# Kernel optimization log

Measured on AMD Instinct MI355X. Metric: run time of the kernel, lower is better.

Reference implementation:

```python
import jax, jax.numpy as jnp
import numpy as np

FP8_MAX = 448.0  # max normal of float8_e4m3fn (TE fwd format)
EPS = 1e-12


def _fp8_quant_dequant(t):
    """Per-tensor amax scaling -> cast to e4m3 -> dequant back to f32.
    Mirrors TE's per-tensor scaling recipe (scale = FP8_MAX / amax)."""
    amax = jnp.max(jnp.abs(t))
    scale = FP8_MAX / jnp.maximum(amax, EPS)
    q = jnp.clip(t * scale, -FP8_MAX, FP8_MAX).astype(jnp.float8_e4m3fn)
    return q.astype(jnp.float32) / scale


def setup_inputs() -> dict:
    key = jax.random.key(0)
    k1, k2, k3 = jax.random.split(key, 3)
    tokens, d_in, d_out = 8192, 4096, 4096
    x = jax.random.normal(k1, (tokens, d_in), dtype=jnp.float32)
    # kaiming_uniform_(a=sqrt(5)) -> U(-bound, bound), bound = sqrt(6/((1+a^2)*fan_in)) = 1/sqrt(fan_in)
    bound = 1.0 / np.sqrt(d_in)
    weight = jax.random.uniform(k2, (d_out, d_in), dtype=jnp.float32, minval=-bound, maxval=bound)
    bias = jnp.zeros((d_out,), dtype=jnp.float32) + 0.01 * jax.random.normal(k3, (d_out,), dtype=jnp.float32)
    return {"x": x, "weight": weight, "bias": bias}


def reference(x, weight, bias):
    # fp8 quant/dequant of activations and weights, then GEMM + bias
    xq = _fp8_quant_dequant(x)            # [T, Din]
    wq = _fp8_quant_dequant(weight)       # [Dout, Din]
    out = jnp.einsum("ti,oi->to", xq, wq) # [T, Dout]
    return out + bias[None, :]
```

## Files before the change

### kernel.cpp

```cpp
#include <hip/hip_runtime.h>
#include <stdint.h>

#define M_DIM 8192
#define N_DIM 4096
#define K_DIM 4096

typedef float f32x4  __attribute__((ext_vector_type(4)));
typedef float f32x16 __attribute__((ext_vector_type(16)));
typedef int   i32x4  __attribute__((ext_vector_type(4)));
typedef int   i32x8  __attribute__((ext_vector_type(8)));

__global__ __launch_bounds__(256) void amax2_kernel(const float* __restrict__ x,
                                                    const float* __restrict__ wgt,
                                                    unsigned int* __restrict__ ws_u) {
    const int which = blockIdx.y;
    const float4* p = (const float4*)(which ? wgt : x);
    const int n4 = (which ? N_DIM : M_DIM) * (K_DIM / 4);
    int tid = blockIdx.x * blockDim.x + threadIdx.x;
    int stride = gridDim.x * blockDim.x;
    float m = 0.0f;
    for (int i = tid; i < n4; i += stride) {
        float4 v = p[i];
        m = fmaxf(m, fmaxf(fmaxf(fabsf(v.x), fabsf(v.y)),
                           fmaxf(fabsf(v.z), fabsf(v.w))));
    }
#pragma unroll
    for (int off = 32; off > 0; off >>= 1)
        m = fmaxf(m, __shfl_down(m, off, 64));
    __shared__ float sm[4];
    if ((threadIdx.x & 63) == 0) sm[threadIdx.x >> 6] = m;
    __syncthreads();
    if (threadIdx.x == 0) {
        m = fmaxf(fmaxf(sm[0], sm[1]), fmaxf(sm[2], sm[3]));
        atomicMax(ws_u + which, __float_as_uint(m));
    }
}

__global__ __launch_bounds__(256) void quant2_kernel(const float* __restrict__ x,
                                                     const float* __restrict__ wgt,
                                                     unsigned int* __restrict__ xq,
                                                     unsigned int* __restrict__ wq,
                                                     const unsigned int* __restrict__ ws_u) {
    const int which = blockIdx.y;
    const float4* p = (const float4*)(which ? wgt : x);
    unsigned int* outp = which ? wq : xq;
    const int n4 = (which ? N_DIM : M_DIM) * (K_DIM / 4);
    float amax = fmaxf(__uint_as_float(ws_u[which]), 1e-12f);
    float scale = 448.0f / amax;
    int tid = blockIdx.x * blockDim.x + threadIdx.x;
    int stride = gridDim.x * blockDim.x;
    for (int i = tid; i < n4; i += stride) {
        float4 v = p[i];
        float a = fminf(fmaxf(v.x * scale, -448.0f), 448.0f);
        float b = fminf(fmaxf(v.y * scale, -448.0f), 448.0f);
        float c = fminf(fmaxf(v.z * scale, -448.0f), 448.0f);
        float d = fminf(fmaxf(v.w * scale, -448.0f), 448.0f);
        int w = __builtin_amdgcn_cvt_pk_fp8_f32(a, b, 0, false);
        w = __builtin_amdgcn_cvt_pk_fp8_f32(c, d, w, true);
        outp[i] = (unsigned int)w;
    }
}

__device__ __forceinline__ void gld16(const void* g, void* l) {
    __builtin_amdgcn_global_load_lds(
        (const __attribute__((address_space(1))) void*)g,
        (__attribute__((address_space(3))) void*)l, 16, 0, 0);
}

#define MFMA32(a, b, c) __builtin_amdgcn_mfma_scale_f32_32x32x64_f8f6f4( \
    (a), (b), (c), 0, 0, 0, 0x7F7F7F7F, 0, 0x7F7F7F7F)
#define BAR()    __builtin_amdgcn_s_barrier()
#define VMCNT(n) asm volatile("s_waitcnt vmcnt(" #n ")" ::: "memory")
#define PRIO1()  __builtin_amdgcn_s_setprio(1)
#define PRIO0()  __builtin_amdgcn_s_setprio(0)
#define FENCE()  asm volatile("" ::: "memory")

__global__ __launch_bounds__(256, 1) void gemm_fp8_kernel(
    const uint8_t* __restrict__ Aq,
    const uint8_t* __restrict__ Bq,
    const float* __restrict__ bias,
    const unsigned int* __restrict__ ws_u,
    float* __restrict__ out)
{
    __shared__ uint8_t lds[131072];

    const int tid = threadIdx.x;
    const int w = tid >> 6, l = tid & 63;

    const int cpx = (int)gridDim.x >> 3;
    const int bid = (int)blockIdx.x;
    const int swz = (bid & 7) * cpx + (bid >> 3);
    const int bm = swz >> 4, bn = swz & 15;

    const uint8_t* gA = Aq + (size_t)bm * 256 * K_DIM;
    const uint8_t* gB = Bq + (size_t)bn * 256 * K_DIM;

    const int idx = tid >> 3, p = tid & 7;
    const int srcX = ((p ^ (idx & 7)) << 4);
    const uint8_t* aRow = gA + (size_t)idx * K_DIM + srcX;
    const uint8_t* bRow = gB + (size_t)idx * K_DIM + srcX;
    const int dA = tid * 16;

    const int wr = w >> 1, wc = w & 1;
    const int lr = l & 31;
    const int hi2 = (l >> 5) << 1;
    const int rowA0 = wr * 128 + lr;
    const int rowB0 = wc * 128 + lr;

    auto stageA = [&](int bb, int kn, int half) {
#pragma unroll
        for (int r = 0; r < 4; ++r)
            gld16(aRow + (size_t)(half * 128 + r * 32) * K_DIM + kn,
                  &lds[bb * 32768 + half * 16384 + r * 4096 + dA]);
    };
    auto stageB = [&](int bb, int kn, int half) {
#pragma unroll
        for (int r = 0; r < 4; ++r)
            gld16(bRow + (size_t)(half * 128 + r * 32) * K_DIM + kn,
                  &lds[65536 + bb * 32768 + half * 16384 + r * 4096 + dA]);
    };
    auto ldf = [&](const uint8_t* base, int row, int kh) -> i32x8 {
        const uint8_t* q = base + (row << 7);
        const int rk = row & 7;
        const int c0 = (kh << 2) + hi2;
        i32x4 lo = *(const i32x4*)(q + ((c0 ^ rk) << 4));
        i32x4 hh = *(const i32x4*)(q + (((c0 + 1) ^ rk) << 4));
        return __builtin_shufflevector(lo, hh, 0, 1, 2, 3, 4, 5, 6, 7);
    };

    f32x16 acc[4][4] = {};
    i32x8 av[4], bv[4];

    stageA(0, 0, 0); stageB(0, 0, 0);
    stageA(0, 0, 1); stageB(0, 0, 1);

    for (int t = 0; t < 32; ++t) {
        const int buf = t & 1, nbuf = buf ^ 1;
        const int kn = (t + 1) * 128;
        const uint8_t* lab = &lds[buf * 32768];
        const uint8_t* lbb = &lds[65536 + buf * 32768];

        VMCNT(0);
        BAR();

        if (t < 31) { stageA(nbuf, kn, 0); stageB(nbuf, kn, 0); }
        bv[0] = ldf(lbb, rowB0, 0);      bv[1] = ldf(lbb, rowB0 + 32, 0);
        av[0] = ldf(lab, rowA0, 0);      av[1] = ldf(lab, rowA0 + 32, 0);
        av[2] = ldf(lab, rowA0 + 64, 0); av[3] = ldf(lab, rowA0 + 96, 0);
        PRIO1();
        acc[0][0] = MFMA32(av[0], bv[0], acc[0][0]);
        acc[0][1] = MFMA32(av[0], bv[1], acc[0][1]);
        acc[1][0] = MFMA32(av[1], bv[0], acc[1][0]);
        acc[1][1] = MFMA32(av[1], bv[1], acc[1][1]);
        acc[2][0] = MFMA32(av[2], bv[0], acc[2][0]);
        acc[2][1] = MFMA32(av[2], bv[1], acc[2][1]);
        acc[3][0] = MFMA32(av[3], bv[0], acc[3][0]);
        acc[3][1] = MFMA32(av[3], bv[1], acc[3][1]);
        PRIO0();
        FENCE();

        if (t < 31) { stageA(nbuf, kn, 1); stageB(nbuf, kn, 1); }
        bv[2] = ldf(lbb, rowB0 + 64, 0); bv[3] = ldf(lbb, rowB0 + 96, 0);
        PRIO1();
        acc[0][2] = MFMA32(av[0], bv[2], acc[0][2]);
        acc[0][3] = MFMA32(av[0], bv[3], acc[0][3]);
        acc[1][2] = MFMA32(av[1], bv[2], acc[1][2]);
        acc[1][3] = MFMA32(av[1], bv[3], acc[1][3]);
        acc[2][2] = MFMA32(av[2], bv[2], acc[2][2]);
        acc[2][3] = MFMA32(av[2], bv[3], acc[2][3]);
        acc[3][2] = MFMA32(av[3], bv[2], acc[3][2]);
        acc[3][3] = MFMA32(av[3], bv[3], acc[3][3]);
        PRIO0();
        FENCE();

        av[0] = ldf(lab, rowA0, 1);      av[1] = ldf(lab, rowA0 + 32, 1);
        av[2] = ldf(lab, rowA0 + 64, 1); av[3] = ldf(lab, rowA0 + 96, 1);
        bv[0] = ldf(lbb, rowB0, 1);      bv[1] = ldf(lbb, rowB0 + 32, 1);
        PRIO1();
        acc[0][0] = MFMA32(av[0], bv[0], acc[0][0]);
        acc[0][1] = MFMA32(av[0], bv[1], acc[0][1]);
        acc[1][0] = MFMA32(av[1], bv[0], acc[1][0]);
        acc[1][1] = MFMA32(av[1], bv[1], acc[1][1]);
        acc[2][0] = MFMA32(av[2], bv[0], acc[2][0]);
        acc[2][1] = MFMA32(av[2], bv[1], acc[2][1]);
        acc[3][0] = MFMA32(av[3], bv[0], acc[3][0]);
        acc[3][1] = MFMA32(av[3], bv[1], acc[3][1]);
        PRIO0();
        FENCE();

        bv[2] = ldf(lbb, rowB0 + 64, 1); bv[3] = ldf(lbb, rowB0 + 96, 1);
        PRIO1();
        acc[0][2] = MFMA32(av[0], bv[2], acc[0][2]);
        acc[0][3] = MFMA32(av[0], bv[3], acc[0][3]);
        acc[1][2] = MFMA32(av[1], bv[2], acc[1][2]);
        acc[1][3] = MFMA32(av[1], bv[3], acc[1][3]);
        acc[2][2] = MFMA32(av[2], bv[2], acc[2][2]);
        acc[2][3] = MFMA32(av[2], bv[3], acc[2][3]);
        acc[3][2] = MFMA32(av[3], bv[2], acc[3][2]);
        acc[3][3] = MFMA32(av[3], bv[3], acc[3][3]);
        PRIO0();
    }

    const float ax = fmaxf(__uint_as_float(ws_u[0]), 1e-12f);
    const float aw = fmaxf(__uint_as_float(ws_u[1]), 1e-12f);
    const float inv = (ax * (1.0f / 448.0f)) * (aw * (1.0f / 448.0f));

    const int orow0 = bm * 256 + wr * 128 + ((l >> 5) << 2);
    const int ocol0 = bn * 256 + wc * 128 + lr;
#pragma unroll
    for (int mb = 0; mb < 4; ++mb) {
#pragma unroll
        for (int nb = 0; nb < 4; ++nb) {
            const int col = ocol0 + nb * 32;
            const float bvv = bias[col];
#pragma unroll
            for (int r = 0; r < 16; ++r) {
                const int row = orow0 + mb * 32 + (r & 3) + ((r >> 2) << 3);
                out[(size_t)row * N_DIM + col] = acc[mb][nb][r] * inv + bvv;
            }
        }
    }
}

extern "C" void kernel_launch(void* const* d_in, const int* in_sizes, int n_in,
                              void* d_out, int out_size, void* d_ws, size_t ws_size,
                              hipStream_t stream) {
    const float* x    = (const float*)d_in[0];
    const float* wgt  = (const float*)d_in[1];
    const float* bias = (const float*)d_in[2];
    float* out = (float*)d_out;

    unsigned int* ws_u = (unsigned int*)d_ws;
    uint8_t* xq = (uint8_t*)d_ws + 256;
    uint8_t* wq = xq + (size_t)M_DIM * K_DIM;

    hipMemsetAsync(d_ws, 0, 8, stream);

    dim3 ga(1024, 2);
    amax2_kernel<<<ga, 256, 0, stream>>>(x, wgt, ws_u);

    dim3 gq(2048, 2);
    quant2_kernel<<<gq, 256, 0, stream>>>(x, wgt, (unsigned int*)xq,
                                          (unsigned int*)wq, ws_u);

    gemm_fp8_kernel<<<(M_DIM / 256) * (N_DIM / 256), 256, 0, stream>>>(
        xq, wq, bias, ws_u, out);
}
```

Baseline: 215.8 us.

## Software-pipeline LDS fragment loads across iterations with split register sets

Restructures the GEMM main loop so the next tile's first A/B fragments are read from LDS before the last MFMA group of the current iteration. Separate register sets per k-half let loads overlap with MFMAs. All global-to-LDS staging for the next buffer is now issued up front, and the barrier moves to the end of the iteration. The cost is higher register pressure, and the earlier barrier placement could expose more wait time on global loads.

```diff
diff --git a/kernel.cpp b/kernel.cpp
--- a/kernel.cpp
+++ b/kernel.cpp
@@ -71,9 +71,9 @@
     (a), (b), (c), 0, 0, 0, 0x7F7F7F7F, 0, 0x7F7F7F7F)
 #define BAR()    __builtin_amdgcn_s_barrier()
 #define VMCNT(n) asm volatile("s_waitcnt vmcnt(" #n ")" ::: "memory")
+#define LGKM0()  asm volatile("s_waitcnt lgkmcnt(0)" ::: "memory")
 #define PRIO1()  __builtin_amdgcn_s_setprio(1)
 #define PRIO0()  __builtin_amdgcn_s_setprio(0)
-#define FENCE()  asm volatile("" ::: "memory")
 
 __global__ __launch_bounds__(256, 1) void gemm_fp8_kernel(
     const uint8_t* __restrict__ Aq,
@@ -129,75 +129,84 @@
     };
 
     f32x16 acc[4][4] = {};
-    i32x8 av[4], bv[4];
+    i32x8 a0[4], a1[4], b00[2], b01[2], b10[2], b11[2];
 
     stageA(0, 0, 0); stageB(0, 0, 0);
     stageA(0, 0, 1); stageB(0, 0, 1);
+    VMCNT(0); BAR();
+    a0[0] = ldf(&lds[0], rowA0, 0);       a0[1] = ldf(&lds[0], rowA0 + 32, 0);
+    a0[2] = ldf(&lds[0], rowA0 + 64, 0);  a0[3] = ldf(&lds[0], rowA0 + 96, 0);
+    b00[0] = ldf(&lds[65536], rowB0, 0);  b00[1] = ldf(&lds[65536], rowB0 + 32, 0);
 
     for (int t = 0; t < 32; ++t) {
-        const int buf = t & 1, nbuf = buf ^ 1;
-        const int kn = (t + 1) * 128;
+        const int buf = t & 1;
         const uint8_t* lab = &lds[buf * 32768];
         const uint8_t* lbb = &lds[65536 + buf * 32768];
-
-        VMCNT(0);
-        BAR();
-
-        if (t < 31) { stageA(nbuf, kn, 0); stageB(nbuf, kn, 0); }
-        bv[0] = ldf(lbb, rowB0, 0);      bv[1] = ldf(lbb, rowB0 + 32, 0);
-        av[0] = ldf(lab, rowA0, 0);      av[1] = ldf(lab, rowA0 + 32, 0);
-        av[2] = ldf(lab, rowA0 + 64, 0); av[3] = ldf(lab, rowA0 + 96, 0);
-        PRIO1();
-        acc[0][0] = MFMA32(av[0], bv[0], acc[0][0]);
-        acc[0][1] = MFMA32(av[0], bv[1], acc[0][1]);
-        acc[1][0] = MFMA32(av[1], bv[0], acc[1][0]);
-        acc[1][1] = MFMA32(av[1], bv[1], acc[1][1]);
-        acc[2][0] = MFMA32(av[2], bv[0], acc[2][0]);
-        acc[2][1] = MFMA32(av[2], bv[1], acc[2][1]);
-        acc[3][0] = MFMA32(av[3], bv[0], acc[3][0]);
-        acc[3][1] = MFMA32(av[3], bv[1], acc[3][1]);
-        PRIO0();
-        FENCE();
-
-        if (t < 31) { stageA(nbuf, kn, 1); stageB(nbuf, kn, 1); }
-        bv[2] = ldf(lbb, rowB0 + 64, 0); bv[3] = ldf(lbb, rowB0 + 96, 0);
-        PRIO1();
-        acc[0][2] = MFMA32(av[0], bv[2], acc[0][2]);
-        acc[0][3] = MFMA32(av[0], bv[3], acc[0][3]);
-        acc[1][2] = MFMA32(av[1], bv[2], acc[1][2]);
-        acc[1][3] = MFMA32(av[1], bv[3], acc[1][3]);
-        acc[2][2] = MFMA32(av[2], bv[2], acc[2][2]);
-        acc[2][3] = MFMA32(av[2], bv[3], acc[2][3]);
-        acc[3][2] = MFMA32(av[3], bv[2], acc[3][2]);
-        acc[3][3] = MFMA32(av[3], bv[3], acc[3][3]);
-        PRIO0();
-        FENCE();
-
-        av[0] = ldf(lab, rowA0, 1);      av[1] = ldf(lab, rowA0 + 32, 1);
-        av[2] = ldf(lab, rowA0 + 64, 1); av[3] = ldf(lab, rowA0 + 96, 1);
-        bv[0] = ldf(lbb, rowB0, 1);      bv[1] = ldf(lbb, rowB0 + 32, 1);
-        PRIO1();
-        acc[0][0] = MFMA32(av[0], bv[0], acc[0][0]);
-        acc[0][1] = MFMA32(av[0], bv[1], acc[0][1]);
-        acc[1][0] = MFMA32(av[1], bv[0], acc[1][0]);
-        acc[1][1] = MFMA32(av[1], bv[1], acc[1][1]);
-        acc[2][0] = MFMA32(av[2], bv[0], acc[2][0]);
-        acc[2][1] = MFMA32(av[2], bv[1], acc[2][1]);
-        acc[3][0] = MFMA32(av[3], bv[0], acc[3][0]);
-        acc[3][1] = MFMA32(av[3], bv[1], acc[3][1]);
-        PRIO0();
-        FENCE();
-
-        bv[2] = ldf(lbb, rowB0 + 64, 1); bv[3] = ldf(lbb, rowB0 + 96, 1);
-        PRIO1();
-        acc[0][2] = MFMA32(av[0], bv[2], acc[0][2]);
-        acc[0][3] = MFMA32(av[0], bv[3], acc[0][3]);
-        acc[1][2] = MFMA32(av[1], bv[2], acc[1][2]);
-        acc[1][3] = MFMA32(av[1], bv[3], acc[1][3]);
-        acc[2][2] = MFMA32(av[2], bv[2], acc[2][2]);
-        acc[2][3] = MFMA32(av[2], bv[3], acc[2][3]);
-        acc[3][2] = MFMA32(av[3], bv[2], acc[3][2]);
-        acc[3][3] = MFMA32(av[3], bv[3], acc[3][3]);
+        const int kn = (t + 1) * 128;
+
+        if (t < 31) {
+            stageA(buf ^ 1, kn, 0); stageB(buf ^ 1, kn, 0);
+            stageA(buf ^ 1, kn, 1); stageB(buf ^ 1, kn, 1);
+        }
+
+        b01[0] = ldf(lbb, rowB0 + 64, 0); b01[1] = ldf(lbb, rowB0 + 96, 0);
+        a1[0] = ldf(lab, rowA0, 1);       a1[1] = ldf(lab, rowA0 + 32, 1);
+        a1[2] = ldf(lab, rowA0 + 64, 1);  a1[3] = ldf(lab, rowA0 + 96, 1);
+        PRIO1();
+        acc[0][0] = MFMA32(a0[0], b00[0], acc[0][0]);
+        acc[0][1] = MFMA32(a0[0], b00[1], acc[0][1]);
+        acc[1][0] = MFMA32(a0[1], b00[0], acc[1][0]);
+        acc[1][1] = MFMA32(a0[1], b00[1], acc[1][1]);
+        acc[2][0] = MFMA32(a0[2], b00[0], acc[2][0]);
+        acc[2][1] = MFMA32(a0[2], b00[1], acc[2][1]);
+        acc[3][0] = MFMA32(a0[3], b00[0], acc[3][0]);
+        acc[3][1] = MFMA32(a0[3], b00[1], acc[3][1]);
+        PRIO0();
+
+        b10[0] = ldf(lbb, rowB0, 1);      b10[1] = ldf(lbb, rowB0 + 32, 1);
+        PRIO1();
+        acc[0][2] = MFMA32(a0[0], b01[0], acc[0][2]);
+        acc[0][3] = MFMA32(a0[0], b01[1], acc[0][3]);
+        acc[1][2] = MFMA32(a0[1], b01[0], acc[1][2]);
+        acc[1][3] = MFMA32(a0[1], b01[1], acc[1][3]);
+        acc[2][2] = MFMA32(a0[2], b01[0], acc[2][2]);
+        acc[2][3] = MFMA32(a0[2], b01[1], acc[2][3]);
+        acc[3][2] = MFMA32(a0[3], b01[0], acc[3][2]);
+        acc[3][3] = MFMA32(a0[3], b01[1], acc[3][3]);
+        PRIO0();
+
+        b11[0] = ldf(lbb, rowB0 + 64, 1); b11[1] = ldf(lbb, rowB0 + 96, 1);
+        PRIO1();
+        acc[0][0] = MFMA32(a1[0], b10[0], acc[0][0]);
+        acc[0][1] = MFMA32(a1[0], b10[1], acc[0][1]);
+        acc[1][0] = MFMA32(a1[1], b10[0], acc[1][0]);
+        acc[1][1] = MFMA32(a1[1], b10[1], acc[1][1]);
+        acc[2][0] = MFMA32(a1[2], b10[0], acc[2][0]);
+        acc[2][1] = MFMA32(a1[2], b10[1], acc[2][1]);
+        acc[3][0] = MFMA32(a1[3], b10[0], acc[3][0]);
+        acc[3][1] = MFMA32(a1[3], b10[1], acc[3][1]);
+        PRIO0();
+
+        if (t < 31) {
+            LGKM0();
+            VMCNT(0);
+            BAR();
+            const uint8_t* nlab = &lds[(buf ^ 1) * 32768];
+            const uint8_t* nlbb = &lds[65536 + (buf ^ 1) * 32768];
+            a0[0] = ldf(nlab, rowA0, 0);      a0[1] = ldf(nlab, rowA0 + 32, 0);
+            a0[2] = ldf(nlab, rowA0 + 64, 0); a0[3] = ldf(nlab, rowA0 + 96, 0);
+            b00[0] = ldf(nlbb, rowB0, 0);     b00[1] = ldf(nlbb, rowB0 + 32, 0);
+        }
+
+        PRIO1();
+        acc[0][2] = MFMA32(a1[0], b11[0], acc[0][2]);
+        acc[0][3] = MFMA32(a1[0], b11[1], acc[0][3]);
+        acc[1][2] = MFMA32(a1[1], b11[0], acc[1][2]);
+        acc[1][3] = MFMA32(a1[1], b11[1], acc[1][3]);
+        acc[2][2] = MFMA32(a1[2], b11[0], acc[2][2]);
+        acc[2][3] = MFMA32(a1[2], b11[1], acc[2][3]);
+        acc[3][2] = MFMA32(a1[3], b11[0], acc[3][2]);
+        acc[3][3] = MFMA32(a1[3], b11[1], acc[3][3]);
         PRIO0();
     }
 
```

New measurement: 229.2 us. 1.06x slower.
